# Optimization experiments

Measured on AMD Instinct MI355X. Metric: run time of the kernel, lower is better.

Reference implementation:

```python
import math
import jax, jax.numpy as jnp
import numpy as np

B, T, D = 8, 2048, 512
EPS = 1e-5


def _gate(x, W, b, a, g, beta):
    # Linear -> PReLU (single shared slope a) -> LayerNorm -> sigmoid
    h = x @ W.T + b
    h = jnp.where(h >= 0, h, a * h)
    mu = jnp.mean(h, axis=-1, keepdims=True)
    var = jnp.var(h, axis=-1, keepdims=True)
    h = (h - mu) / jnp.sqrt(var + EPS) * g + beta
    return jax.nn.sigmoid(h)


def setup_inputs() -> dict:
    key = jax.random.key(0)
    ks = jax.random.split(key, 12)
    lin = lambda k: jax.random.normal(k, (D, D), jnp.float32) * 0.02
    z = jnp.zeros((D,), jnp.float32)
    o = jnp.ones((D,), jnp.float32)
    a0 = jnp.float32(0.25)  # PReLU default init
    inp = {
        "query": jax.random.normal(ks[0], (B, T, D), jnp.float32),
        "value": jax.random.normal(ks[1], (B, T, D), jnp.float32),
        "aux_emb": jax.random.normal(ks[2], (B, 1, D), jnp.float32),
        # ragged valid lengths in [T//2, T] to keep every sample realistic
        "input_len": jax.random.randint(ks[3], (B,), T // 2, T + 1),
        "Wq": lin(ks[4]), "bq": z,
        "Wqg": lin(ks[5]), "bqg": z, "aq": a0, "gq": o, "betaq": z,
        "Wkg": lin(ks[6]), "bkg": z, "ak": a0, "gk": o, "betak": z,
        "Wvg": lin(ks[7]), "bvg": z, "av": a0, "gv": o, "betav": z,
        "Wsig": lin(ks[8]), "bsig": z,
        "Wtan": lin(ks[9]), "btan": z,
    }
    return inp


def reference(query, value, aux_emb, input_len,
              Wq, bq,
              Wqg, bqg, aq, gq, betaq,
              Wkg, bkg, ak, gk, betak,
              Wvg, bvg, av, gv, betav,
              Wsig, bsig, Wtan, btan):
    q = query @ Wq.T + bq
    q = q * _gate(aux_emb, Wqg, bqg, aq, gq, betaq)          # [B,T,D]
    k = value * _gate(aux_emb, Wkg, bkg, ak, gk, betak)      # [B,T,D]
    vg = _gate(aux_emb, Wvg, bvg, av, gv, betav)             # [B,1,D]
    vg = jax.nn.sigmoid(vg @ Wsig.T + bsig) * jnp.tanh(vg @ Wtan.T + btan)
    v = value * vg                                           # [B,T,D]

    w = jnp.einsum('btd,bsd->bts', q, k) / math.sqrt(D)      # [B,T,T]
    r = jnp.arange(T)
    causal = (r[:, None] >= r[None, :]).astype(w.dtype)      # tril ones
    w = w * causal
    w = jnp.where(w == 0.0, -jnp.inf, w)  # torch quirk: exact zeros -> -inf
    L = input_len[:, None, None]                              # [B,1,1]
    invalid = (r[None, :, None] < L) & (r[None, None, :] >= L)
    w = jnp.where(invalid, -jnp.inf, w)
    p = jax.nn.softmax(w, axis=-1)
    # rows beyond input_len are padding: zero them (torch code produced NaN
    # there via -inf*0; intended semantics is zeroed padding rows)
    row_valid = (r[None, :, None] < L).astype(p.dtype)        # [B,T,1]
    p = p * row_valid
    return p @ v                                              # [B,T,D]
```

## Files before the change

kernel.cpp:

```cpp
#include <hip/hip_runtime.h>
#include <hip/hip_bf16.h>
#include <stdint.h>

#define BB 8
#define TT 2048
#define DD 512

typedef __attribute__((ext_vector_type(8))) __bf16 bf16x8;
typedef __attribute__((ext_vector_type(4))) float f32x4;

__device__ __forceinline__ unsigned short f2bf(float f) {
    unsigned u = __builtin_bit_cast(unsigned, f);
    unsigned r = u + 0x7fffu + ((u >> 16) & 1u);
    return (unsigned short)(r >> 16);
}

__device__ __forceinline__ void gload_lds16(const unsigned short* g, unsigned short* l) {
    __builtin_amdgcn_global_load_lds(
        (const __attribute__((address_space(1))) void*)g,
        (__attribute__((address_space(3))) void*)l, 16, 0, 0);
}

__global__ __launch_bounds__(256) void gates_mv1(
    const float* __restrict__ aux,
    const float* __restrict__ Wqg, const float* __restrict__ bqg, const float* __restrict__ aq,
    const float* __restrict__ Wkg, const float* __restrict__ bkg, const float* __restrict__ ak,
    const float* __restrict__ Wvg, const float* __restrict__ bvg, const float* __restrict__ av,
    float* __restrict__ h) {
    __shared__ float saux[BB * DD];
    int tid = threadIdx.x;
#pragma unroll
    for (int i = 0; i < 4; i++) {
        int idx = tid + i * 256;
        ((float4*)saux)[idx] = ((const float4*)aux)[idx];
    }
    __syncthreads();
    int wave = (blockIdx.x * 256 + tid) >> 6;
    int lane = tid & 63;
    int g = wave >> 9, r = wave & 511;
    const float* W    = (g == 0) ? Wqg : (g == 1) ? Wkg : Wvg;
    const float* bias = (g == 0) ? bqg : (g == 1) ? bkg : bvg;
    const float* alpha = (g == 0) ? aq : (g == 1) ? ak : av;
    const float4* Wrow = (const float4*)(W + (size_t)r * DD);
    float acc[BB];
#pragma unroll
    for (int b = 0; b < BB; b++) acc[b] = 0.f;
#pragma unroll
    for (int c = 0; c < 2; c++) {
        float4 w4 = Wrow[lane + c * 64];
#pragma unroll
        for (int b = 0; b < BB; b++) {
            float4 a4 = ((const float4*)(saux + b * DD))[lane + c * 64];
            acc[b] += w4.x * a4.x + w4.y * a4.y + w4.z * a4.z + w4.w * a4.w;
        }
    }
#pragma unroll
    for (int b = 0; b < BB; b++) {
#pragma unroll
        for (int s = 1; s < 64; s <<= 1) acc[b] += __shfl_xor(acc[b], s, 64);
    }
    if (lane == 0) {
        float bi = bias[r], a = alpha[0];
#pragma unroll
        for (int b = 0; b < BB; b++) {
            float v = acc[b] + bi;
            v = (v >= 0.f) ? v : a * v;
            h[(g * BB + b) * DD + r] = v;
        }
    }
}

__global__ __launch_bounds__(512) void gates_norm(
    const float* __restrict__ h,
    const float* __restrict__ gq, const float* __restrict__ betaq,
    const float* __restrict__ gk, const float* __restrict__ betak,
    const float* __restrict__ gv, const float* __restrict__ betav,
    float* __restrict__ qgate, float* __restrict__ kgate, float* __restrict__ vg) {
    int g = blockIdx.x >> 3, b = blockIdx.x & 7, tid = threadIdx.x;
    __shared__ float red[DD], red2[DD];
    float hv = h[(g * BB + b) * DD + tid];
    red[tid] = hv; red2[tid] = hv * hv;
    __syncthreads();
    for (int s = 256; s > 0; s >>= 1) {
        if (tid < s) { red[tid] += red[tid + s]; red2[tid] += red2[tid + s]; }
        __syncthreads();
    }
    float mu = red[0] * (1.f / DD);
    float var = red2[0] * (1.f / DD) - mu * mu;
    const float* gg = (g == 0) ? gq : (g == 1) ? gk : gv;
    const float* be = (g == 0) ? betaq : (g == 1) ? betak : betav;
    float val = (hv - mu) * rsqrtf(var + 1e-5f) * gg[tid] + be[tid];
    float sg = 1.f / (1.f + expf(-val));
    float* outp = (g == 0) ? qgate : (g == 1) ? kgate : vg;
    outp[b * DD + tid] = sg;
}

__global__ __launch_bounds__(256) void gates_mv2(
    const float* __restrict__ vg,
    const float* __restrict__ Wsig, const float* __restrict__ bsig,
    const float* __restrict__ Wtan, const float* __restrict__ btan,
    float* __restrict__ vgate) {
    __shared__ float svg[BB * DD];
    int tid = threadIdx.x;
#pragma unroll
    for (int i = 0; i < 4; i++) {
        int idx = tid + i * 256;
        ((float4*)svg)[idx] = ((const float4*)vg)[idx];
    }
    __syncthreads();
    int r = (blockIdx.x * 256 + tid) >> 6;
    int lane = tid & 63;
    const float4* Ws = (const float4*)(Wsig + (size_t)r * DD);
    const float4* Wt = (const float4*)(Wtan + (size_t)r * DD);
    float as_[BB], at_[BB];
#pragma unroll
    for (int b = 0; b < BB; b++) { as_[b] = 0.f; at_[b] = 0.f; }
#pragma unroll
    for (int c = 0; c < 2; c++) {
        float4 w1 = Ws[lane + c * 64];
        float4 w2 = Wt[lane + c * 64];
#pragma unroll
        for (int b = 0; b < BB; b++) {
            float4 a4 = ((const float4*)(svg + b * DD))[lane + c * 64];
            as_[b] += w1.x * a4.x + w1.y * a4.y + w1.z * a4.z + w1.w * a4.w;
            at_[b] += w2.x * a4.x + w2.y * a4.y + w2.z * a4.z + w2.w * a4.w;
        }
    }
#pragma unroll
    for (int b = 0; b < BB; b++) {
#pragma unroll
        for (int s = 1; s < 64; s <<= 1) {
            as_[b] += __shfl_xor(as_[b], s, 64);
            at_[b] += __shfl_xor(at_[b], s, 64);
        }
    }
    if (lane == 0) {
        float b1 = bsig[r], b2 = btan[r];
#pragma unroll
        for (int b = 0; b < BB; b++) {
            float s1 = 1.f / (1.f + expf(-(as_[b] + b1)));
            float s2 = tanhf(at_[b] + b2);
            vgate[b * DD + r] = s1 * s2;
        }
    }
}

__global__ __launch_bounds__(256) void convert_kernel(
    const float* __restrict__ query, const float* __restrict__ Wq,
    const float* __restrict__ value,
    const float* __restrict__ kgate, const float* __restrict__ vgate,
    unsigned short* __restrict__ queryb, unsigned short* __restrict__ Wqb,
    unsigned short* __restrict__ kb, unsigned short* __restrict__ vbT) {
    __shared__ float tile[32][33];
    int bi = blockIdx.x, tid = threadIdx.x;
    if (bi < 8192) {
        int idx = bi * 256 + tid;
        float4 q4 = ((const float4*)query)[idx];
        ushort4 oq;
        oq.x = f2bf(q4.x); oq.y = f2bf(q4.y); oq.z = f2bf(q4.z); oq.w = f2bf(q4.w);
        ((ushort4*)queryb)[idx] = oq;
    } else if (bi < 8448) {
        int idx = (bi - 8192) * 256 + tid;
        float4 w4 = ((const float4*)Wq)[idx];
        ushort4 o;
        o.x = f2bf(w4.x); o.y = f2bf(w4.y); o.z = f2bf(w4.z); o.w = f2bf(w4.w);
        ((ushort4*)Wqb)[idx] = o;
    } else {
        int vb = bi - 8448;
        int tIdx = vb & 63, dIdx = (vb >> 6) & 15, b = vb >> 10;
        int t0 = tIdx * 32, d0 = dIdx * 32;
        int tx = tid & 31, ty = tid >> 5;
        float kg = kgate[b * DD + d0 + tx];
#pragma unroll
        for (int i = 0; i < 4; i++) {
            int t = t0 + ty + i * 8;
            float v = value[((size_t)b * TT + t) * DD + d0 + tx];
            tile[ty + i * 8][tx] = v;
            kb[((size_t)b * TT + t) * DD + d0 + tx] = f2bf(v * kg);
        }
        __syncthreads();
#pragma unroll
        for (int i = 0; i < 4; i++) {
            int d = d0 + ty + i * 8;
            float g = vgate[b * DD + d];
            vbT[((size_t)b * DD + d) * TT + t0 + tx] = f2bf(tile[tx][ty + i * 8] * g);
        }
    }
}

#define GEMM_CORE(APTR, ALDA, BPTR, BLDA, KSTART, KEND)                                   \
    __shared__ __align__(16) unsigned short As[128 * 32];                                 \
    __shared__ __align__(16) unsigned short Bs[128 * 32];                                 \
    int tid = threadIdx.x;                                                                \
    int lane = tid & 63, wid = tid >> 6;                                                  \
    int wm = (wid >> 1) * 64, wn = (wid & 1) * 64;                                        \
    int lm = lane & 15, quad = lane >> 4;                                                 \
    f32x4 acc[4][4];                                                                      \
    _Pragma("unroll") for (int im = 0; im < 4; im++)                                      \
        _Pragma("unroll") for (int in = 0; in < 4; in++)                                  \
            acc[im][in] = (f32x4){0.f, 0.f, 0.f, 0.f};                                    \
    for (int k0 = (KSTART); k0 < (KEND); k0 += 32) {                                      \
        _Pragma("unroll") for (int i = 0; i < 2; i++) {                                   \
            int idx = tid * 8 + i * 2048;                                                 \
            int r = idx >> 5;                                                             \
            int cg = ((idx >> 3) & 3) ^ ((r >> 1) & 3);                                   \
            gload_lds16(&(APTR)[(size_t)r * (ALDA) + k0 + cg * 8], &As[idx]);             \
            gload_lds16(&(BPTR)[(size_t)r * (BLDA) + k0 + cg * 8], &Bs[idx]);             \
        }                                                                                 \
        __syncthreads();                                                                  \
        bf16x8 af[4], bf_[4];                                                             \
        _Pragma("unroll") for (int i = 0; i < 4; i++) {                                   \
            int row = wm + i * 16 + lm;                                                   \
            af[i] = *(const bf16x8*)&As[row * 32 + (quad ^ ((row >> 1) & 3)) * 8];        \
        }                                                                                 \
        _Pragma("unroll") for (int i = 0; i < 4; i++) {                                   \
            int row = wn + i * 16 + lm;                                                   \
            bf_[i] = *(const bf16x8*)&Bs[row * 32 + (quad ^ ((row >> 1) & 3)) * 8];       \
        }                                                                                 \
        _Pragma("unroll") for (int im = 0; im < 4; im++)                                  \
            _Pragma("unroll") for (int in = 0; in < 4; in++)                              \
                acc[im][in] = __builtin_amdgcn_mfma_f32_16x16x32_bf16(af[im], bf_[in],    \
                                                                     acc[im][in], 0, 0, 0);\
        __syncthreads();                                                                  \
    }

__global__ __launch_bounds__(256) void qgemm_kernel(
    const unsigned short* __restrict__ Amat, const unsigned short* __restrict__ Bmat,
    const float* __restrict__ bq, const float* __restrict__ qgate,
    unsigned short* __restrict__ qb) {
    int m0 = blockIdx.x * 128, n0 = blockIdx.y * 128;
    const unsigned short* Ap = Amat + (size_t)m0 * DD;
    const unsigned short* Bp = Bmat + (size_t)n0 * DD;
    GEMM_CORE(Ap, DD, Bp, DD, 0, DD)
    int b = m0 >> 11;
#pragma unroll
    for (int im = 0; im < 4; im++) {
        int row = m0 + wm + im * 16 + quad * 4;
#pragma unroll
        for (int in = 0; in < 4; in++) {
            int col = n0 + wn + in * 16 + lm;
            float bias = bq[col];
            float g = qgate[b * DD + col];
#pragma unroll
            for (int r = 0; r < 4; r++) {
                float v = (acc[im][in][r] + bias) * g;
                qb[(size_t)(row + r) * DD + col] = f2bf(v);
            }
        }
    }
}

__global__ __launch_bounds__(256) void scores_kernel(
    const unsigned short* __restrict__ qb, const unsigned short* __restrict__ kb,
    unsigned short* __restrict__ P, float* __restrict__ rowsum) {
    int b = blockIdx.z;
    int idx = blockIdx.x;
    int mt = (int)((sqrtf(8.f * idx + 1.f) - 1.f) * 0.5f);
    while ((mt + 1) * (mt + 2) / 2 <= idx) mt++;
    while (mt * (mt + 1) / 2 > idx) mt--;
    int nt = idx - mt * (mt + 1) / 2;
    int t0 = mt * 128, s0 = nt * 128;
    const unsigned short* Ap = qb + ((size_t)b * TT + t0) * DD;
    const unsigned short* Bp = kb + ((size_t)b * TT + s0) * DD;
    GEMM_CORE(Ap, DD, Bp, DD, 0, DD)
    const float scale = 0.044194173824159216f;
    unsigned short* Ptile = P + ((size_t)b * 136 + (size_t)mt * (mt + 1) / 2 + nt) * 16384;
#pragma unroll
    for (int im = 0; im < 4; im++) {
        int ltb = wm + im * 16 + quad * 4;
        float rs[4] = {0.f, 0.f, 0.f, 0.f};
#pragma unroll
        for (int in = 0; in < 4; in++) {
            int ls = wn + in * 16 + lm;
            int s = s0 + ls;
#pragma unroll
            for (int r = 0; r < 4; r++) {
                float p = (s <= t0 + ltb + r) ? expf(acc[im][in][r] * scale) : 0.f;
                Ptile[(size_t)(ltb + r) * 128 + ls] = f2bf(p);
                rs[r] += p;
            }
        }
#pragma unroll
        for (int r = 0; r < 4; r++) {
            float v = rs[r];
            v += __shfl_xor(v, 1, 64);
            v += __shfl_xor(v, 2, 64);
            v += __shfl_xor(v, 4, 64);
            v += __shfl_xor(v, 8, 64);
            if (lm == 0) atomicAdd(&rowsum[b * TT + t0 + ltb + r], v);
        }
    }
}

__global__ __launch_bounds__(256) void out_kernel(
    const unsigned short* __restrict__ P, const unsigned short* __restrict__ vbT,
    const float* __restrict__ rowsum, const int* __restrict__ input_len,
    float* __restrict__ out) {
    int nt = blockIdx.x;
    int pr = blockIdx.y;
    int b = blockIdx.z;
    int n0 = nt * 128;
    int L = input_len[b];

    __shared__ __align__(16) unsigned short As[128 * 32];
    __shared__ __align__(16) unsigned short Bs[128 * 32];
    int tid = threadIdx.x;
    int lane = tid & 63, wid = tid >> 6;
    int wm = (wid >> 1) * 64, wn = (wid & 1) * 64;
    int lm = lane & 15, quad = lane >> 4;

#pragma unroll
    for (int half = 0; half < 2; half++) {
        int mt = half ? (15 - pr) : pr;
        int t0 = mt * 128;
        size_t triBase = ((size_t)b * 136 + (size_t)mt * (mt + 1) / 2) * 16384;
        int kend = (mt + 1) * 128;

        f32x4 acc[4][4];
#pragma unroll
        for (int im = 0; im < 4; im++)
#pragma unroll
            for (int in = 0; in < 4; in++) acc[im][in] = (f32x4){0.f, 0.f, 0.f, 0.f};

        for (int k0 = 0; k0 < kend; k0 += 32) {
#pragma unroll
            for (int i = 0; i < 2; i++) {
                int idx = tid * 8 + i * 2048;
                int r = idx >> 5;
                int cg = ((idx >> 3) & 3) ^ ((r >> 1) & 3);
                const unsigned short* ag = P + triBase + (size_t)(k0 >> 7) * 16384 +
                                           (size_t)r * 128 + (k0 & 127) + cg * 8;
                gload_lds16(ag, &As[idx]);
                gload_lds16(&vbT[(size_t)(b * DD + n0 + r) * TT + k0 + cg * 8], &Bs[idx]);
            }
            __syncthreads();
            bf16x8 af[4], bf_[4];
#pragma unroll
            for (int i = 0; i < 4; i++) {
                int row = wm + i * 16 + lm;
                af[i] = *(const bf16x8*)&As[row * 32 + (quad ^ ((row >> 1) & 3)) * 8];
            }
#pragma unroll
            for (int i = 0; i < 4; i++) {
                int row = wn + i * 16 + lm;
                bf_[i] = *(const bf16x8*)&Bs[row * 32 + (quad ^ ((row >> 1) & 3)) * 8];
            }
#pragma unroll
            for (int im = 0; im < 4; im++)
#pragma unroll
                for (int in = 0; in < 4; in++)
                    acc[im][in] = __builtin_amdgcn_mfma_f32_16x16x32_bf16(af[im], bf_[in],
                                                                         acc[im][in], 0, 0, 0);
            __syncthreads();
        }

#pragma unroll
        for (int im = 0; im < 4; im++) {
            int tbase = t0 + wm + im * 16 + quad * 4;
#pragma unroll
            for (int r = 0; r < 4; r++) {
                int t = tbase + r;
                float inv = 1.f / rowsum[b * TT + t];
                bool valid = (t < L);
#pragma unroll
                for (int in = 0; in < 4; in++) {
                    int n = n0 + wn + in * 16 + lm;
                    float o = valid ? acc[im][in][r] * inv : 0.f;
                    out[((size_t)b * TT + t) * DD + n] = o;
                }
            }
        }
    }
}

extern "C" void kernel_launch(void* const* d_in, const int* in_sizes, int n_in,
                              void* d_out, int out_size, void* d_ws, size_t ws_size,
                              hipStream_t stream) {
    const float* query = (const float*)d_in[0];
    const float* value = (const float*)d_in[1];
    const float* aux   = (const float*)d_in[2];
    const int*   ilen  = (const int*)d_in[3];
    const float* Wq    = (const float*)d_in[4];
    const float* bq    = (const float*)d_in[5];
    const float* Wqg   = (const float*)d_in[6];
    const float* bqg   = (const float*)d_in[7];
    const float* aq    = (const float*)d_in[8];
    const float* gq    = (const float*)d_in[9];
    const float* betaq = (const float*)d_in[10];
    const float* Wkg   = (const float*)d_in[11];
    const float* bkg   = (const float*)d_in[12];
    const float* ak    = (const float*)d_in[13];
    const float* gk    = (const float*)d_in[14];
    const float* betak = (const float*)d_in[15];
    const float* Wvg   = (const float*)d_in[16];
    const float* bvg   = (const float*)d_in[17];
    const float* av    = (const float*)d_in[18];
    const float* gv    = (const float*)d_in[19];
    const float* betav = (const float*)d_in[20];
    const float* Wsig  = (const float*)d_in[21];
    const float* bsig  = (const float*)d_in[22];
    const float* Wtan  = (const float*)d_in[23];
    const float* btan  = (const float*)d_in[24];

    char* ws = (char*)d_ws;
    float* qgate          = (float*)(ws + 0);
    float* kgate          = (float*)(ws + 16384);
    float* vgate          = (float*)(ws + 32768);
    float* rowsum         = (float*)(ws + 49152);
    unsigned short* Wqb   = (unsigned short*)(ws + 114688);
    unsigned short* queryb= (unsigned short*)(ws + 638976);
    unsigned short* qb    = (unsigned short*)(ws + 17416192);
    unsigned short* kb    = (unsigned short*)(ws + 34193408);
    unsigned short* vbT   = (unsigned short*)(ws + 50970624);
    unsigned short* P     = (unsigned short*)(ws + 67747840);
    float* hbuf           = (float*)(ws + 67747840);
    float* vg             = (float*)(ws + 67747840 + 49152);

    hipMemsetAsync(rowsum, 0, BB * TT * sizeof(float), stream);

    gates_mv1<<<384, 256, 0, stream>>>(aux, Wqg, bqg, aq, Wkg, bkg, ak, Wvg, bvg, av, hbuf);
    gates_norm<<<24, 512, 0, stream>>>(hbuf, gq, betaq, gk, betak, gv, betav,
                                       qgate, kgate, vg);
    gates_mv2<<<128, 256, 0, stream>>>(vg, Wsig, bsig, Wtan, btan, vgate);

    convert_kernel<<<16640, 256, 0, stream>>>(query, Wq, value, kgate, vgate,
                                              queryb, Wqb, kb, vbT);
    qgemm_kernel<<<dim3((BB * TT) / 128, DD / 128), 256, 0, stream>>>(queryb, Wqb, bq, qgate, qb);
    scores_kernel<<<dim3(136, 1, BB), 256, 0, stream>>>(qb, kb, P, rowsum);
    out_kernel<<<dim3(4, 8, BB), 256, 0, stream>>>(P, vbT, rowsum, ilen, (float*)d_out);
}
```

Before: 293.5 us.

## Retile P@V kernel to 64-row M tiles with 64-wide K steps

The output GEMM (P@V) now uses 64-row M tiles instead of 128, with a 64-element K step per iteration, a matching 8-way XOR swizzle, and twice as many blocks in the grid (16 pairs of triangular row tiles). The causal K range is cut at 64-row granularity, which removes wasted work on the triangle. Halving K iterations reduces barrier count, and more blocks improve occupancy across CUs. In exchange each block does fewer MFMAs per loaded B tile, so V is reloaded twice as often.

```diff
diff --git a/kernel.cpp b/kernel.cpp
--- a/kernel.cpp
+++ b/kernel.cpp
@@ -302,60 +302,78 @@
     int n0 = nt * 128;
     int L = input_len[b];
 
-    __shared__ __align__(16) unsigned short As[128 * 32];
-    __shared__ __align__(16) unsigned short Bs[128 * 32];
+    __shared__ __align__(16) unsigned short As[64 * 64];
+    __shared__ __align__(16) unsigned short Bs[128 * 64];
     int tid = threadIdx.x;
     int lane = tid & 63, wid = tid >> 6;
-    int wm = (wid >> 1) * 64, wn = (wid & 1) * 64;
+    int wm = (wid >> 1) * 32, wn = (wid & 1) * 64;
     int lm = lane & 15, quad = lane >> 4;
 
 #pragma unroll
     for (int half = 0; half < 2; half++) {
-        int mt = half ? (15 - pr) : pr;
-        int t0 = mt * 128;
-        size_t triBase = ((size_t)b * 136 + (size_t)mt * (mt + 1) / 2) * 16384;
-        int kend = (mt + 1) * 128;
-
-        f32x4 acc[4][4];
-#pragma unroll
-        for (int im = 0; im < 4; im++)
+        int mt = half ? (31 - pr) : pr;
+        int t0 = mt * 64;
+        int mt128 = mt >> 1;
+        int rowoff = (mt & 1) * 64;
+        size_t triBase = ((size_t)b * 136 + (size_t)mt128 * (mt128 + 1) / 2) * 16384;
+        int ksteps = mt + 1;
+
+        f32x4 acc[2][4];
+#pragma unroll
+        for (int im = 0; im < 2; im++)
 #pragma unroll
             for (int in = 0; in < 4; in++) acc[im][in] = (f32x4){0.f, 0.f, 0.f, 0.f};
 
-        for (int k0 = 0; k0 < kend; k0 += 32) {
+        for (int ks = 0; ks < ksteps; ks++) {
+            int k0 = ks * 64;
+            int stile = k0 >> 7;
+            int coloff = k0 & 64;
 #pragma unroll
             for (int i = 0; i < 2; i++) {
                 int idx = tid * 8 + i * 2048;
-                int r = idx >> 5;
-                int cg = ((idx >> 3) & 3) ^ ((r >> 1) & 3);
-                const unsigned short* ag = P + triBase + (size_t)(k0 >> 7) * 16384 +
-                                           (size_t)r * 128 + (k0 & 127) + cg * 8;
+                int r = idx >> 6;
+                int c = (idx >> 3) & 7;
+                int cs = c ^ (r & 7);
+                const unsigned short* ag = P + triBase + (size_t)stile * 16384 +
+                                           (size_t)(rowoff + r) * 128 + coloff + cs * 8;
                 gload_lds16(ag, &As[idx]);
-                gload_lds16(&vbT[(size_t)(b * DD + n0 + r) * TT + k0 + cg * 8], &Bs[idx]);
+            }
+#pragma unroll
+            for (int i = 0; i < 4; i++) {
+                int idx = tid * 8 + i * 2048;
+                int r = idx >> 6;
+                int c = (idx >> 3) & 7;
+                int cs = c ^ (r & 7);
+                gload_lds16(&vbT[(size_t)(b * DD + n0 + r) * TT + k0 + cs * 8], &Bs[idx]);
             }
             __syncthreads();
-            bf16x8 af[4], bf_[4];
-#pragma unroll
-            for (int i = 0; i < 4; i++) {
-                int row = wm + i * 16 + lm;
-                af[i] = *(const bf16x8*)&As[row * 32 + (quad ^ ((row >> 1) & 3)) * 8];
-            }
-#pragma unroll
-            for (int i = 0; i < 4; i++) {
-                int row = wn + i * 16 + lm;
-                bf_[i] = *(const bf16x8*)&Bs[row * 32 + (quad ^ ((row >> 1) & 3)) * 8];
-            }
-#pragma unroll
-            for (int im = 0; im < 4; im++)
-#pragma unroll
-                for (int in = 0; in < 4; in++)
-                    acc[im][in] = __builtin_amdgcn_mfma_f32_16x16x32_bf16(af[im], bf_[in],
-                                                                         acc[im][in], 0, 0, 0);
+            bf16x8 af[2][2], bf_[4][2];
+#pragma unroll
+            for (int kk = 0; kk < 2; kk++) {
+#pragma unroll
+                for (int i = 0; i < 2; i++) {
+                    int row = wm + i * 16 + lm;
+                    af[i][kk] = *(const bf16x8*)&As[row * 64 + ((kk * 4 + quad) ^ (row & 7)) * 8];
+                }
+#pragma unroll
+                for (int i = 0; i < 4; i++) {
+                    int row = wn + i * 16 + lm;
+                    bf_[i][kk] = *(const bf16x8*)&Bs[row * 64 + ((kk * 4 + quad) ^ (row & 7)) * 8];
+                }
+            }
+#pragma unroll
+            for (int kk = 0; kk < 2; kk++)
+#pragma unroll
+                for (int im = 0; im < 2; im++)
+#pragma unroll
+                    for (int in = 0; in < 4; in++)
+                        acc[im][in] = __builtin_amdgcn_mfma_f32_16x16x32_bf16(
+                            af[im][kk], bf_[in][kk], acc[im][in], 0, 0, 0);
             __syncthreads();
         }
 
 #pragma unroll
-        for (int im = 0; im < 4; im++) {
+        for (int im = 0; im < 2; im++) {
             int tbase = t0 + wm + im * 16 + quad * 4;
 #pragma unroll
             for (int r = 0; r < 4; r++) {
@@ -427,5 +445,5 @@
                                               queryb, Wqb, kb, vbT);
     qgemm_kernel<<<dim3((BB * TT) / 128, DD / 128), 256, 0, stream>>>(queryb, Wqb, bq, qgate, qb);
     scores_kernel<<<dim3(136, 1, BB), 256, 0, stream>>>(qb, kb, P, rowsum);
-    out_kernel<<<dim3(4, 8, BB), 256, 0, stream>>>(P, vbT, rowsum, ilen, (float*)d_out);
-}
+    out_kernel<<<dim3(4, 16, BB), 256, 0, stream>>>(P, vbT, rowsum, ilen, (float*)d_out);
+}
```

New measurement: 275.1 us. 1.07x faster.
